# Kernel tuning notes

Hardware: AMD Instinct MI355X
Metric: run time of the kernel (lower is better)

The kernel has to match this reference:

```python
import jax, jax.numpy as jnp
from jax import lax
import numpy as np

N_SPLITS = 2
N_LEVELS = 3
B, T, C = 32, 1024, 128
HID = 512          # int(input_dim * hidden_size) = 128 * 4
K1, K2 = 5, 3      # first conv kernel_size, second conv kernel=3
N_INTER = 7        # 1 + 2 + 4 interactors in the binary tree
LEAKY_SLOPE = 0.01


def setup_inputs() -> dict:
    key = jax.random.key(0)
    ks = jax.random.split(key, 9)
    w = 0.05  # small init so exp-gating stays well-conditioned
    return {
        "x": jax.random.normal(ks[0], (B, T, C), jnp.float32),
        "mul_w1": jax.random.normal(ks[1], (N_INTER, N_SPLITS, K1, C, HID), jnp.float32) * w,
        "mul_b1": jnp.zeros((N_INTER, N_SPLITS, HID), jnp.float32),
        "mul_w2": jax.random.normal(ks[2], (N_INTER, N_SPLITS, K2, HID, C), jnp.float32) * w,
        "mul_b2": jnp.zeros((N_INTER, N_SPLITS, C), jnp.float32),
        "add_w1": jax.random.normal(ks[3], (N_INTER, N_SPLITS, K1, C, HID), jnp.float32) * w,
        "add_b1": jnp.zeros((N_INTER, N_SPLITS, HID), jnp.float32),
        "add_w2": jax.random.normal(ks[4], (N_INTER, N_SPLITS, K2, HID, C), jnp.float32) * w,
        "add_b2": jnp.zeros((N_INTER, N_SPLITS, C), jnp.float32),
    }


def _leaky(x):
    return jnp.where(x > 0, x, LEAKY_SLOPE * x)


def _causal_conv(x, w, b):
    # x: [B, L, Cin], w: [K, Cin, Cout] (keras WIO layout); 'causal' = left-pad K-1
    k = w.shape[0]
    y = lax.conv_general_dilated(x, w, window_strides=(1,),
                                 padding=[(k - 1, 0)],
                                 dimension_numbers=("NWC", "WIO", "NWC"))
    return y + b


def _conv_seq(x, w1, b1, w2, b2):
    # Conv1D(causal, LeakyReLU 0.01) -> Dropout(identity at inference) -> Conv1D(k=3, causal, tanh)
    h = _leaky(_causal_conv(x, w1, b1))
    return jnp.tanh(_causal_conv(h, w2, b2))


def _interactor(x, idx, p):
    # x: [B, L, C]; strided temporal split into N_SPLITS pieces of length L//N_SPLITS
    splits = [x[:, i::N_SPLITS, :] for i in range(N_SPLITS)]
    scale = N_SPLITS - 1
    mul_list = []
    for i in range(N_SPLITS):
        s = 0.0
        for j in range(N_SPLITS):
            if j != i:
                s = s + _conv_seq(splits[j], p["mul_w1"][idx, i], p["mul_b1"][idx, i],
                                  p["mul_w2"][idx, i], p["mul_b2"][idx, i])
        # prod_j exp(f(x_j)) ** (1/scale) == exp(sum_j f(x_j) / scale)
        mul_list.append(splits[i] * jnp.exp(s / scale))
    out = []
    for i in range(N_SPLITS):
        a = 0.0
        for j in range(N_SPLITS):
            if j != i:
                a = a + _conv_seq(mul_list[j], p["add_w1"][idx, i], p["add_b1"][idx, i],
                                  p["add_w2"][idx, i], p["add_b2"][idx, i])
        a = a / scale
        out.append(mul_list[i] + a if i % 2 == 0 else mul_list[i] - a)
    return out


def reference(x, mul_w1, mul_b1, mul_w2, mul_b2, add_w1, add_b1, add_w2, add_b2):
    p = {"mul_w1": mul_w1, "mul_b1": mul_b1, "mul_w2": mul_w2, "mul_b2": mul_b2,
         "add_w1": add_w1, "add_b1": add_b1, "add_w2": add_w2, "add_b2": add_b2}
    t_in = x.shape[1]
    min_unit = N_SPLITS ** N_LEVELS
    pad = (-t_in) % min_unit  # left zero-pad to a multiple of n_splits**n_levels
    xp = jnp.pad(x, ((0, 0), (pad, 0), (0, 0)))
    seq = [xp]
    idx = 0
    for lvl in range(N_LEVELS):
        nxt = []
        for j in range(N_SPLITS ** lvl):
            nxt += _interactor(seq[j], idx, p)
            idx += 1
        seq = nxt
    # rev_split: recursively concatenate along time with stride `steps`
    while len(seq) > 1:
        steps = len(seq) // N_SPLITS
        seq = [jnp.concatenate([seq[i + s * steps] for s in range(N_SPLITS)], axis=1)
               for i in range(steps)]
    return seq[0][:, -t_in:, :]
```

## Files before the change

### kernel.cpp

```cpp
#include <hip/hip_runtime.h>
#include <hip/hip_bf16.h>
#include <stdint.h>


static constexpr int B_ = 32, T_ = 1024, C_ = 128, HID_ = 512;
static constexpr int K1_ = 5, K2_ = 3;

typedef __attribute__((ext_vector_type(8))) _Float16 half8;
typedef __attribute__((ext_vector_type(4))) float f32x4;

__device__ __forceinline__ unsigned short f2h(float f) {
    _Float16 h = (_Float16)f;
    return __builtin_bit_cast(unsigned short, h);
}

__device__ __forceinline__ void gload16(const void* g, void* l) {
    __builtin_amdgcn_global_load_lds(
        (const __attribute__((address_space(1))) unsigned int*)g,
        (__attribute__((address_space(3))) unsigned int*)l, 16, 0, 0);
}

template<int CIN, int COUT, bool SWZ>
__global__ __launch_bounds__(256)
void wprep_k(const float* __restrict__ win1, unsigned short* __restrict__ wout1,
             const float* __restrict__ win2, unsigned short* __restrict__ wout2,
             int nhalf) {
    constexpr int TA = CIN / 64, TB = COUT / 64;
    int blk = blockIdx.x;
    int tb = blk % TB;
    int ta = (blk / TB) % TA;
    int s  = blk / (TA * TB);
    const float* win;
    unsigned short* wout;
    if (s < nhalf) { win = win1; wout = wout1; }
    else           { win = win2; wout = wout2; s -= nhalf; }
    __shared__ float tile[64][65];
    const float* src = win + (size_t)s * CIN * COUT;
    unsigned short* dst = wout + (size_t)s * CIN * COUT;
    int cl = threadIdx.x & 63;
    int rw = threadIdx.x >> 6;
    for (int r = rw; r < 64; r += 4)
        tile[r][cl] = src[(size_t)(ta * 64 + r) * COUT + tb * 64 + cl];
    __syncthreads();
    for (int r = rw; r < 64; r += 4) {
        int co = tb * 64 + r;
        int ci = ta * 64 + cl;
        int ciw = SWZ ? ((ci & ~127) | ((ci & 127) ^ ((co & 7) << 3))) : ci;
        dst[(size_t)co * CIN + ciw] = f2h(tile[cl][r]);
    }
}

__global__ __launch_bounds__(256)
void split_k(const float* __restrict__ cur, unsigned short* __restrict__ outb,
             int Ls) {
    int idx = blockIdx.x * 256 + threadIdx.x;
    int row = idx >> 5;
    int cq  = (idx & 31) << 2;
    int BLs = B_ * Ls;
    int g  = row / BLs;
    int r2 = row - g * BLs;
    int b  = r2 / Ls;
    int u  = r2 - b * Ls;
    int p = g >> 1, i = g & 1;
    const float4 v = *(const float4*)(cur +
        ((size_t)(p * B_ + b) * (2 * Ls) + 2 * u + i) * C_ + cq);
    ushort4 o;
    o.x = f2h(v.x); o.y = f2h(v.y); o.z = f2h(v.z); o.w = f2h(v.w);
    int cqw = cq ^ (((u + 4) & 7) << 3);
    *(ushort4*)(outb + (size_t)row * C_ + cqw) = o;
}

__global__ __launch_bounds__(256, 2)
void conv1_k(const unsigned short* __restrict__ actb,
             const unsigned short* __restrict__ wL,
             const float* __restrict__ bias,
             unsigned short* __restrict__ hid,
             const unsigned short* __restrict__ zp,
             int Ls, int rsplit, int idxbase) {
    __shared__ unsigned short smemA[2][80 * 128];

    const int tid = threadIdx.x;
    const int lane = tid & 63;
    const int w = tid >> 6;
    const int wr = w >> 1, wc = w & 1;

    const int blk = blockIdx.x;
    const int ct = blk & 7;
    const int rs = (blk >> 3) % rsplit;
    const int g  = (blk >> 3) / rsplit;
    const int n0 = ct * 64;
    const int gin  = g ^ 1;
    const int widx = (idxbase + (g >> 1)) * 2 + (g & 1);

    const char* gbase = (const char*)(actb + (size_t)gin * B_ * Ls * C_);
    const float* bptr = bias + (size_t)widx * HID_;

    const unsigned short* wlane = wL + (size_t)widx * (K1_ * HID_ * C_)
        + (size_t)(n0 + wc * 32 + (lane & 15)) * C_ + ((lane >> 4) << 3);
    half8 breg[K1_][2][4];
#pragma unroll
    for (int t = 0; t < K1_; ++t)
#pragma unroll
        for (int n = 0; n < 2; ++n)
#pragma unroll
            for (int ks = 0; ks < 4; ++ks)
                breg[t][n][ks] = *(const half8*)(wlane
                    + ((size_t)t * HID_ + n * 16) * C_ + ks * 32);

    const float bv0 = bptr[n0 + wc * 32 + (lane & 15)];
    const float bv1 = bptr[n0 + wc * 32 + 16 + (lane & 15)];

    const int rtbase = rs * 8;
    const int i0 = ct & 7;

    auto stage = [&](int rt, int p) {
        const int b  = (rt * 64) / Ls;
        const int t0 = (rt * 64) % Ls;
        const char* inb = gbase + (size_t)b * Ls * 256;
#pragma unroll
        for (int j = 0; j < 5; ++j) {
            int ch = w * 5 + j;
            int q = ch * 1024 + lane * 16;
            int r = q >> 8;
            int cb = q & 255;
            int t = t0 - 4 + r;
            const char* src = (t >= 0) ? inb + (size_t)t * 256 + cb
                                       : (const char*)zp + cb;
            gload16(src, (char*)smemA[p] + ch * 1024);
        }
    };

    stage(rtbase + i0, 0);
    asm volatile("s_waitcnt vmcnt(0)" ::: "memory");
    __syncthreads();

#pragma unroll
    for (int i = 0; i < 8; ++i) {
        const int rt = rtbase + ((i + i0) & 7);
        const int b  = (rt * 64) / Ls;
        const int t0 = (rt * 64) % Ls;
        const int p  = i & 1;

        __syncthreads();
        if (i < 7) stage(rtbase + ((i + 1 + i0) & 7), p ^ 1);
        if (i > 0) {
            if (i < 7) {
                asm volatile("s_waitcnt vmcnt(21)" ::: "memory");
            } else {
                asm volatile("s_waitcnt vmcnt(16)" ::: "memory");
            }
            __syncthreads();
        }

        f32x4 acc[2][2];
#pragma unroll
        for (int m = 0; m < 2; ++m)
#pragma unroll
            for (int n = 0; n < 2; ++n) acc[m][n] = (f32x4){0.f, 0.f, 0.f, 0.f};

        const unsigned short* sA = smemA[p];
#pragma unroll
        for (int kk = 0; kk < K1_; ++kk) {
#pragma unroll
            for (int ks = 0; ks < 4; ++ks) {
                half8 aF[2];
                const int cole = ks * 32 + ((lane >> 4) << 3);
#pragma unroll
                for (int m = 0; m < 2; ++m) {
                    int ar = kk + wr * 32 + m * 16 + (lane & 15);
                    aF[m] = *(const half8*)(sA + ar * 128 + (cole ^ ((ar & 7) << 3)));
                }
#pragma unroll
                for (int m = 0; m < 2; ++m) {
                    acc[m][0] = __builtin_amdgcn_mfma_f32_16x16x32_f16(
                        aF[m], breg[kk][0][ks], acc[m][0], 0, 0, 0);
                    acc[m][1] = __builtin_amdgcn_mfma_f32_16x16x32_f16(
                        aF[m], breg[kk][1][ks], acc[m][1], 0, 0, 0);
                }
            }
        }

        unsigned short* outp = hid + ((size_t)(g * B_ + b) * Ls + t0) * HID_;
#pragma unroll
        for (int n = 0; n < 2; ++n) {
            const int co = n0 + wc * 32 + n * 16 + (lane & 15);
            const float bv = n ? bv1 : bv0;
#pragma unroll
            for (int m = 0; m < 2; ++m) {
                const int u0 = wr * 32 + m * 16 + ((lane >> 4) << 2);
#pragma unroll
                for (int q = 0; q < 4; ++q) {
                    float v = acc[m][n][q] + bv;
                    v = (v > 0.f) ? v : 0.01f * v;
                    int t = t0 + u0 + q;
                    int cow = (co & ~127) | ((co & 127) ^ (((t + 2) & 7) << 3));
                    outp[(size_t)(u0 + q) * HID_ + cow] = f2h(v);
                }
            }
        }
    }
}

template<int EPI>
__global__ __launch_bounds__(256, 3)
void conv2_k(const unsigned short* __restrict__ hid,
             const unsigned short* __restrict__ wT,
             const float* __restrict__ bias,
             const float* __restrict__ cur,
             float* __restrict__ mulf,
             unsigned short* __restrict__ actb,
             float* __restrict__ nxt,
             unsigned short* __restrict__ actn,
             float* __restrict__ dout,
             const unsigned short* __restrict__ zp,
             int Ls, int RT, int idxbase) {
    __shared__ unsigned short smemA[66 * 128];
    __shared__ unsigned short smemB[128 * 128];

    const int tid = threadIdx.x;
    const int lane = tid & 63;
    const int w = tid >> 6;
    const int wr = w >> 1, wc = w & 1;

    int blk = blockIdx.x;
    const int rt = blk % RT;
    const int g  = blk / RT;
    const int rowstart = rt * 64;
    const int b  = rowstart / Ls;
    const int t0 = rowstart - b * Ls;
    const int widx = (idxbase + (g >> 1)) * 2 + (g & 1);

    const char* inb = (const char*)(hid + (size_t)(g * B_ + b) * Ls * HID_);
    const char* wb  = (const char*)(wT + (size_t)widx * (K2_ * C_ * HID_));
    const float* bptr = bias + (size_t)widx * C_;

    const int c0 = blk & 3;
    const int k0 = blk % 3;

    f32x4 acc[2][4];
#pragma unroll
    for (int m = 0; m < 2; ++m)
#pragma unroll
        for (int n = 0; n < 4; ++n) acc[m][n] = (f32x4){0.f, 0.f, 0.f, 0.f};

    for (int ckp = 0; ckp < 4; ++ckp) {
        const int ck = (ckp + c0) & 3;
        if (ckp) __syncthreads();
        for (int ch = w; ch < 17; ch += 4) {
            int q = ch * 1024 + lane * 16;
            if (q < 16896) {
                int r = q >> 8;
                int cb = q & 255;
                int t = t0 - 2 + r;
                const char* src = (t >= 0)
                    ? inb + (size_t)t * 1024 + ck * 256 + cb
                    : (const char*)zp + cb;
                gload16(src, (char*)smemA + ch * 1024);
            }
        }
        for (int kkp = 0; kkp < K2_; ++kkp) {
            const int kk = (kkp + k0) % 3;
            if (kkp) __syncthreads();
            const char* wt = wb + (size_t)kk * C_ * HID_ * 2;
            for (int ch = w; ch < 32; ch += 4) {
                int q = ch * 1024 + lane * 16;
                int co = q >> 8;
                int cb = q & 255;
                gload16(wt + (size_t)co * 1024 + ck * 256 + cb,
                        (char*)smemB + ch * 1024);
            }
            asm volatile("s_waitcnt vmcnt(0)" ::: "memory");
            __syncthreads();

#pragma unroll
            for (int ks = 0; ks < 4; ++ks) {
                half8 aF[2], bF[4];
                const int cole = ks * 32 + ((lane >> 4) << 3);
#pragma unroll
                for (int m = 0; m < 2; ++m) {
                    int ar = kk + wr * 32 + m * 16 + (lane & 15);
                    aF[m] = *(const half8*)(smemA + ar * 128 + (cole ^ ((ar & 7) << 3)));
                }
#pragma unroll
                for (int n = 0; n < 4; ++n) {
                    int br = wc * 64 + n * 16 + (lane & 15);
                    bF[n] = *(const half8*)(smemB + br * 128 + (cole ^ ((br & 7) << 3)));
                }
#pragma unroll
                for (int m = 0; m < 2; ++m)
#pragma unroll
                    for (int n = 0; n < 4; ++n)
                        acc[m][n] = __builtin_amdgcn_mfma_f32_16x16x32_f16(
                            aF[m], bF[n], acc[m][n], 0, 0, 0);
            }
        }
    }

    const size_t rowb = (size_t)(g * B_ + b) * Ls + t0;
    const int p_ = g >> 1, i_ = g & 1;
    const int Ls2 = Ls >> 1;
#pragma unroll
    for (int n = 0; n < 4; ++n) {
        int c = wc * 64 + n * 16 + (lane & 15);
        float bv = bptr[c];
#pragma unroll
        for (int m = 0; m < 2; ++m) {
            int u0 = wr * 32 + m * 16 + ((lane >> 4) << 2);
#pragma unroll
            for (int q = 0; q < 4; ++q) {
                float v = acc[m][n][q] + bv;
                float xc = fminf(fmaxf(v, -15.f), 15.f);
                float e2 = __expf(2.f * xc);
                float th = (e2 - 1.f) / (e2 + 1.f);
                size_t ro = rowb + (size_t)(u0 + q);
                int u = t0 + u0 + q;
                if (EPI == 0) {
                    float sv = cur[((size_t)(p_ * B_ + b) * (2 * Ls) + 2 * u + i_) * C_ + c];
                    float mv = sv * __expf(th);
                    mulf[ro * C_ + c] = mv;
                    int cw = c ^ (((u + 4) & 7) << 3);
                    actb[ro * C_ + cw] = f2h(mv);
                } else {
                    float mv = mulf[ro * C_ + c];
                    float val = (i_ == 0) ? (mv + th) : (mv - th);
                    if (EPI == 1) {
                        nxt[ro * C_ + c] = val;
                        int gq = g * 2 + (u & 1);
                        int uq = u >> 1;
                        int cw = c ^ (((uq + 4) & 7) << 3);
                        actn[((size_t)(gq * B_ + b) * Ls2 + uq) * C_ + cw] = f2h(val);
                    } else {
                        int tau = u | (((g >> 2) & 1) << 7) | (((g >> 1) & 1) << 8)
                                    | ((g & 1) << 9);
                        dout[((size_t)b * T_ + tau) * C_ + c] = val;
                    }
                }
            }
        }
    }
}

extern "C" void kernel_launch(void* const* d_in, const int* in_sizes, int n_in,
                              void* d_out, int out_size, void* d_ws, size_t ws_size,
                              hipStream_t stream) {
    const float* x   = (const float*)d_in[0];
    const float* mw1 = (const float*)d_in[1];
    const float* mb1 = (const float*)d_in[2];
    const float* mw2 = (const float*)d_in[3];
    const float* mb2 = (const float*)d_in[4];
    const float* aw1 = (const float*)d_in[5];
    const float* ab1 = (const float*)d_in[6];
    const float* aw2 = (const float*)d_in[7];
    const float* ab2 = (const float*)d_in[8];

    char* ws = (char*)d_ws;
    size_t off = 0;
    auto alloc = [&](size_t sz) {
        char* p = ws + off;
        off += (sz + 255) & ~(size_t)255;
        return p;
    };
    unsigned short* zp   = (unsigned short*)alloc(8192);
    unsigned short* w1m  = (unsigned short*)alloc((size_t)14 * 5 * 512 * 128 * 2);
    unsigned short* w1a  = (unsigned short*)alloc((size_t)14 * 5 * 512 * 128 * 2);
    unsigned short* w2m  = (unsigned short*)alloc((size_t)14 * 3 * 128 * 512 * 2);
    unsigned short* w2a  = (unsigned short*)alloc((size_t)14 * 3 * 128 * 512 * 2);
    float* bufA          = (float*)alloc((size_t)4194304 * 4);
    float* bufB          = (float*)alloc((size_t)4194304 * 4);
    unsigned short* actb = (unsigned short*)alloc((size_t)4194304 * 2);
    unsigned short* hidb = (unsigned short*)alloc((size_t)16777216 * 2);
    float* mulf          = (float*)alloc((size_t)4194304 * 4);
    (void)ws_size; (void)n_in; (void)in_sizes; (void)out_size;

    hipMemsetAsync(zp, 0, 8192, stream);

    wprep_k<128, 512, false><<<2240, 256, 0, stream>>>(mw1, w1m, aw1, w1a, 70);
    wprep_k<512, 128, true ><<<1344, 256, 0, stream>>>(mw2, w2m, aw2, w2a, 42);

    split_k<<<4096, 256, 0, stream>>>(x, actb, 512);

    for (int lvl = 0; lvl < 3; ++lvl) {
        const int P = 1 << lvl;
        const int G = 2 * P;
        const int Ls = (1024 >> lvl) >> 1;
        const int idxbase = P - 1;
        const float* cur = (lvl == 0) ? x : ((lvl == 1) ? bufA : bufB);
        float* nxt = (lvl == 1) ? bufB : bufA;
        const int rsplit = (B_ * Ls / 64) / 8;
        const int RT2 = Ls / 2;

        conv1_k<<<512, 256, 0, stream>>>(actb, w1m, mb1, hidb, zp,
                                         Ls, rsplit, idxbase);
        conv2_k<0><<<G * RT2, 256, 0, stream>>>(hidb, w2m, mb2, cur, mulf,
                                                actb, nullptr, nullptr, nullptr,
                                                zp, Ls, RT2, idxbase);
        conv1_k<<<512, 256, 0, stream>>>(actb, w1a, ab1, hidb, zp,
                                         Ls, rsplit, idxbase);
        if (lvl < 2) {
            conv2_k<1><<<G * RT2, 256, 0, stream>>>(hidb, w2a, ab2, nullptr, mulf,
                                                    nullptr, nxt, actb, nullptr,
                                                    zp, Ls, RT2, idxbase);
        } else {
            conv2_k<2><<<G * RT2, 256, 0, stream>>>(hidb, w2a, ab2, nullptr, mulf,
                                                    nullptr, nullptr, nullptr,
                                                    (float*)d_out,
                                                    zp, Ls, RT2, idxbase);
        }
    }
}
```

Before: 370.6 us.

## Halve conv2 weight LDS tile, cache A fragments, and drop fp32 gate buffer

conv2_k now stages the weight tile in two 64-channel halves, which halves smemB and raises the occupancy hint from 3 to 4 blocks per CU. A fragments are loaded into registers once per (ck,kk) and reused across both halves. The separate fp32 mul buffer is removed: the gated value is stored only as swizzled fp16 in a new actg buffer, and the add stage reads it back from there. This cuts global write and read traffic but doubles the number of barrier rounds, raises register use for the cached fragments, and adds fp16 rounding on the residual path.

```diff
diff --git a/kernel.cpp b/kernel.cpp
--- a/kernel.cpp
+++ b/kernel.cpp
@@ -12,6 +12,10 @@
 __device__ __forceinline__ unsigned short f2h(float f) {
     _Float16 h = (_Float16)f;
     return __builtin_bit_cast(unsigned short, h);
+}
+
+__device__ __forceinline__ float h2f(unsigned short u) {
+    return (float)__builtin_bit_cast(_Float16, u);
 }
 
 __device__ __forceinline__ void gload16(const void* g, void* l) {
@@ -202,25 +206,27 @@
 }
 
 template<int EPI>
-__global__ __launch_bounds__(256, 3)
+__global__ __launch_bounds__(256, 4)
 void conv2_k(const unsigned short* __restrict__ hid,
              const unsigned short* __restrict__ wT,
              const float* __restrict__ bias,
              const float* __restrict__ cur,
-             float* __restrict__ mulf,
-             unsigned short* __restrict__ actb,
+             const unsigned short* __restrict__ gate,
+             unsigned short* __restrict__ gout,
              float* __restrict__ nxt,
              unsigned short* __restrict__ actn,
              float* __restrict__ dout,
              const unsigned short* __restrict__ zp,
              int Ls, int RT, int idxbase) {
     __shared__ unsigned short smemA[66 * 128];
-    __shared__ unsigned short smemB[128 * 128];
+    __shared__ unsigned short smemB[64 * 128];
 
     const int tid = threadIdx.x;
     const int lane = tid & 63;
     const int w = tid >> 6;
     const int wr = w >> 1, wc = w & 1;
+    const int hi8 = (lane >> 4) << 3;
+    const int l15 = lane & 15;
 
     int blk = blockIdx.x;
     const int rt = blk % RT;
@@ -234,18 +240,10 @@
     const char* wb  = (const char*)(wT + (size_t)widx * (K2_ * C_ * HID_));
     const float* bptr = bias + (size_t)widx * C_;
 
-    const int c0 = blk & 3;
-    const int k0 = blk % 3;
-
-    f32x4 acc[2][4];
-#pragma unroll
-    for (int m = 0; m < 2; ++m)
-#pragma unroll
-        for (int n = 0; n < 4; ++n) acc[m][n] = (f32x4){0.f, 0.f, 0.f, 0.f};
-
-    for (int ckp = 0; ckp < 4; ++ckp) {
-        const int ck = (ckp + c0) & 3;
-        if (ckp) __syncthreads();
+    const int bco = lane >> 4;
+    const int bcb = l15 * 16;
+
+    auto stageA = [&](int ck) {
         for (int ch = w; ch < 17; ch += 4) {
             int q = ch * 1024 + lane * 16;
             if (q < 16896) {
@@ -258,41 +256,60 @@
                 gload16(src, (char*)smemA + ch * 1024);
             }
         }
-        for (int kkp = 0; kkp < K2_; ++kkp) {
-            const int kk = (kkp + k0) % 3;
-            if (kkp) __syncthreads();
-            const char* wt = wb + (size_t)kk * C_ * HID_ * 2;
-            for (int ch = w; ch < 32; ch += 4) {
-                int q = ch * 1024 + lane * 16;
-                int co = q >> 8;
-                int cb = q & 255;
-                gload16(wt + (size_t)co * 1024 + ck * 256 + cb,
-                        (char*)smemB + ch * 1024);
-            }
-            asm volatile("s_waitcnt vmcnt(0)" ::: "memory");
-            __syncthreads();
-
-#pragma unroll
-            for (int ks = 0; ks < 4; ++ks) {
-                half8 aF[2], bF[4];
-                const int cole = ks * 32 + ((lane >> 4) << 3);
-#pragma unroll
-                for (int m = 0; m < 2; ++m) {
-                    int ar = kk + wr * 32 + m * 16 + (lane & 15);
-                    aF[m] = *(const half8*)(smemA + ar * 128 + (cole ^ ((ar & 7) << 3)));
+    };
+    auto stageB = [&](int ck, int kk, int h) {
+        const char* wt = wb + (size_t)kk * C_ * HID_ * 2;
+#pragma unroll
+        for (int j = 0; j < 4; ++j) {
+            int ch = w * 4 + j;
+            int co = h * 64 + ch * 4 + bco;
+            gload16(wt + (size_t)co * 1024 + ck * 256 + bcb,
+                    (char*)smemB + ch * 1024);
+        }
+    };
+
+    f32x4 acc[2][4];
+#pragma unroll
+    for (int m = 0; m < 2; ++m)
+#pragma unroll
+        for (int n = 0; n < 4; ++n) acc[m][n] = (f32x4){0.f, 0.f, 0.f, 0.f};
+
+    half8 af[2][4];
+
+    for (int r = 0; r < 24; ++r) {
+        const int ck = r / 6, kk = (r / 2) % 3, h = r & 1;
+        if (r) __syncthreads();
+        stageB(ck, kk, h);
+        if ((r % 6) == 0) stageA(ck);
+        asm volatile("s_waitcnt vmcnt(0)" ::: "memory");
+        __syncthreads();
+
+        if (h == 0) {
+#pragma unroll
+            for (int m = 0; m < 2; ++m)
+#pragma unroll
+                for (int ks = 0; ks < 4; ++ks) {
+                    int ar = kk + wr * 32 + m * 16 + l15;
+                    af[m][ks] = *(const half8*)(smemA + ar * 128
+                        + ((ks * 32 + hi8) ^ ((ar & 7) << 3)));
                 }
-#pragma unroll
-                for (int n = 0; n < 4; ++n) {
-                    int br = wc * 64 + n * 16 + (lane & 15);
-                    bF[n] = *(const half8*)(smemB + br * 128 + (cole ^ ((br & 7) << 3)));
-                }
-#pragma unroll
-                for (int m = 0; m < 2; ++m)
-#pragma unroll
-                    for (int n = 0; n < 4; ++n)
-                        acc[m][n] = __builtin_amdgcn_mfma_f32_16x16x32_f16(
-                            aF[m], bF[n], acc[m][n], 0, 0, 0);
-            }
+        }
+
+#pragma unroll
+        for (int ks = 0; ks < 4; ++ks) {
+            half8 bF[2];
+            const int cole = ks * 32 + hi8;
+#pragma unroll
+            for (int n = 0; n < 2; ++n) {
+                int br = wc * 32 + n * 16 + l15;
+                bF[n] = *(const half8*)(smemB + br * 128 + (cole ^ ((br & 7) << 3)));
+            }
+#pragma unroll
+            for (int m = 0; m < 2; ++m)
+#pragma unroll
+                for (int n = 0; n < 2; ++n)
+                    acc[m][h * 2 + n] = __builtin_amdgcn_mfma_f32_16x16x32_f16(
+                        af[m][ks], bF[n], acc[m][h * 2 + n], 0, 0, 0);
         }
     }
 
@@ -300,35 +317,34 @@
     const int p_ = g >> 1, i_ = g & 1;
     const int Ls2 = Ls >> 1;
 #pragma unroll
-    for (int n = 0; n < 4; ++n) {
-        int c = wc * 64 + n * 16 + (lane & 15);
+    for (int nn = 0; nn < 4; ++nn) {
+        int c = (nn >> 1) * 64 + wc * 32 + (nn & 1) * 16 + l15;
         float bv = bptr[c];
 #pragma unroll
         for (int m = 0; m < 2; ++m) {
             int u0 = wr * 32 + m * 16 + ((lane >> 4) << 2);
 #pragma unroll
             for (int q = 0; q < 4; ++q) {
-                float v = acc[m][n][q] + bv;
+                float v = acc[m][nn][q] + bv;
                 float xc = fminf(fmaxf(v, -15.f), 15.f);
                 float e2 = __expf(2.f * xc);
                 float th = (e2 - 1.f) / (e2 + 1.f);
                 size_t ro = rowb + (size_t)(u0 + q);
                 int u = t0 + u0 + q;
+                int cw = c ^ (((u + 4) & 7) << 3);
                 if (EPI == 0) {
                     float sv = cur[((size_t)(p_ * B_ + b) * (2 * Ls) + 2 * u + i_) * C_ + c];
                     float mv = sv * __expf(th);
-                    mulf[ro * C_ + c] = mv;
-                    int cw = c ^ (((u + 4) & 7) << 3);
-                    actb[ro * C_ + cw] = f2h(mv);
+                    gout[ro * C_ + cw] = f2h(mv);
                 } else {
-                    float mv = mulf[ro * C_ + c];
+                    float mv = h2f(gate[ro * C_ + cw]);
                     float val = (i_ == 0) ? (mv + th) : (mv - th);
                     if (EPI == 1) {
                         nxt[ro * C_ + c] = val;
                         int gq = g * 2 + (u & 1);
                         int uq = u >> 1;
-                        int cw = c ^ (((uq + 4) & 7) << 3);
-                        actn[((size_t)(gq * B_ + b) * Ls2 + uq) * C_ + cw] = f2h(val);
+                        int cw2 = c ^ (((uq + 4) & 7) << 3);
+                        actn[((size_t)(gq * B_ + b) * Ls2 + uq) * C_ + cw2] = f2h(val);
                     } else {
                         int tau = u | (((g >> 2) & 1) << 7) | (((g >> 1) & 1) << 8)
                                     | ((g & 1) << 9);
@@ -368,8 +384,8 @@
     float* bufA          = (float*)alloc((size_t)4194304 * 4);
     float* bufB          = (float*)alloc((size_t)4194304 * 4);
     unsigned short* actb = (unsigned short*)alloc((size_t)4194304 * 2);
+    unsigned short* actg = (unsigned short*)alloc((size_t)4194304 * 2);
     unsigned short* hidb = (unsigned short*)alloc((size_t)16777216 * 2);
-    float* mulf          = (float*)alloc((size_t)4194304 * 4);
     (void)ws_size; (void)n_in; (void)in_sizes; (void)out_size;
 
     hipMemsetAsync(zp, 0, 8192, stream);
@@ -380,28 +396,27 @@
     split_k<<<4096, 256, 0, stream>>>(x, actb, 512);
 
     for (int lvl = 0; lvl < 3; ++lvl) {
-        const int P = 1 << lvl;
-        const int G = 2 * P;
+        const int G = 2 << lvl;
         const int Ls = (1024 >> lvl) >> 1;
-        const int idxbase = P - 1;
-        const float* cur = (lvl == 0) ? x : ((lvl == 1) ? bufA : bufB);
-        float* nxt = (lvl == 1) ? bufB : bufA;
+        const int idxbase = (1 << lvl) - 1;
+        const float* curp = (lvl == 0) ? x : ((lvl == 1) ? bufA : bufB);
+        float* nxtp = (lvl == 1) ? bufB : bufA;
         const int rsplit = (B_ * Ls / 64) / 8;
         const int RT2 = Ls / 2;
 
         conv1_k<<<512, 256, 0, stream>>>(actb, w1m, mb1, hidb, zp,
                                          Ls, rsplit, idxbase);
-        conv2_k<0><<<G * RT2, 256, 0, stream>>>(hidb, w2m, mb2, cur, mulf,
-                                                actb, nullptr, nullptr, nullptr,
+        conv2_k<0><<<G * RT2, 256, 0, stream>>>(hidb, w2m, mb2, curp, nullptr,
+                                                actg, nullptr, nullptr, nullptr,
                                                 zp, Ls, RT2, idxbase);
-        conv1_k<<<512, 256, 0, stream>>>(actb, w1a, ab1, hidb, zp,
+        conv1_k<<<512, 256, 0, stream>>>(actg, w1a, ab1, hidb, zp,
                                          Ls, rsplit, idxbase);
         if (lvl < 2) {
-            conv2_k<1><<<G * RT2, 256, 0, stream>>>(hidb, w2a, ab2, nullptr, mulf,
-                                                    nullptr, nxt, actb, nullptr,
+            conv2_k<1><<<G * RT2, 256, 0, stream>>>(hidb, w2a, ab2, nullptr, actg,
+                                                    nullptr, nxtp, actb, nullptr,
                                                     zp, Ls, RT2, idxbase);
         } else {
-            conv2_k<2><<<G * RT2, 256, 0, stream>>>(hidb, w2a, ab2, nullptr, mulf,
+            conv2_k<2><<<G * RT2, 256, 0, stream>>>(hidb, w2a, ab2, nullptr, actg,
                                                     nullptr, nullptr, nullptr,
                                                     (float*)d_out,
                                                     zp, Ls, RT2, idxbase);
```

Result: slower. 607.0 us (+63.8%).
